# Kernel tuning notes

Hardware: AMD Instinct MI355X
Metric: run time of the kernel (lower is better)

## Reference

```python
import jax, jax.numpy as jnp
import numpy as np

N_NODES = 100000
IN_F = 256
OUT_F = 128
N_EDGES = 1600000


def setup_inputs() -> dict:
    key = jax.random.key(0)
    k1, k2, k3, k4 = jax.random.split(key, 4)
    inputs = jax.random.normal(k1, (N_NODES, IN_F), dtype=jnp.float32)
    edge = jax.random.randint(k2, (2, N_EDGES), 0, N_NODES, dtype=jnp.int64)
    # xavier_uniform for weight [in, out]
    bw = float(np.sqrt(6.0 / (IN_F + OUT_F)))
    weight = jax.random.uniform(k3, (IN_F, OUT_F), minval=-bw, maxval=bw, dtype=jnp.float32)
    ba = float(np.sqrt(6.0 / (OUT_F + 1)))
    a = jax.random.uniform(k4, (OUT_F, 1), minval=-ba, maxval=ba, dtype=jnp.float32)
    return {"inputs": inputs, "edge": edge, "weight": weight, "a": a}


def reference(inputs, edge, weight, a):
    # h: [N, out_features]
    h = inputs @ weight
    # edge-wise gather + abs-diff: [E, out_features]
    diff = jnp.abs(h[edge[0]] - h[edge[1]])
    # dot with attention vector a, relu, squeeze -> [E]
    edge_weight = jax.nn.relu((diff @ a).squeeze(-1))
    return (h, edge_weight)
```

## Files before the change

kernel.cpp:

```cpp
#include <hip/hip_runtime.h>
#include <hip/hip_bf16.h>
#include <stdint.h>

typedef __bf16 bf16x8 __attribute__((ext_vector_type(8)));
typedef float  f32x4  __attribute__((ext_vector_type(4)));

#define M_NODES 100000
#define K_IN    256
#define N_OUT   128
#define N_EDGE  1600000

template <bool FULL>
__device__ __forceinline__ void gemm_tile(
    const float* __restrict__ in, float* __restrict__ h,
    __hip_bfloat16* __restrict__ hmir,
    const bf16x8 (&bfrag)[8][2], const int m0, const int lr, const int q,
    const int nb)
{
    f32x4 acc[4][2];
    #pragma unroll
    for (int mt = 0; mt < 4; ++mt)
        #pragma unroll
        for (int nt = 0; nt < 2; ++nt)
            acc[mt][nt] = f32x4{0.f, 0.f, 0.f, 0.f};

    #pragma unroll
    for (int k8 = 0; k8 < 8; ++k8) {
        const int ka = k8 * 32 + q * 8;
        bf16x8 afrag[4];
        #pragma unroll
        for (int mt = 0; mt < 4; ++mt) {
            const int row = m0 + mt * 16 + lr;
            if (FULL || row < M_NODES) {
                const float* ap = in + (size_t)row * K_IN + ka;
                const f32x4 a0 = *(const f32x4*)ap;
                const f32x4 a1 = *(const f32x4*)(ap + 4);
                #pragma unroll
                for (int j = 0; j < 4; ++j) {
                    afrag[mt][j]     = (__bf16)a0[j];
                    afrag[mt][4 + j] = (__bf16)a1[j];
                }
            } else {
                #pragma unroll
                for (int j = 0; j < 8; ++j) afrag[mt][j] = (__bf16)0.f;
            }
        }
        #pragma unroll
        for (int mt = 0; mt < 4; ++mt)
            #pragma unroll
            for (int nt = 0; nt < 2; ++nt)
                acc[mt][nt] = __builtin_amdgcn_mfma_f32_16x16x32_bf16(
                    afrag[mt], bfrag[k8][nt], acc[mt][nt], 0, 0, 0);
    }

    #pragma unroll
    for (int mt = 0; mt < 4; ++mt) {
        const int rb = m0 + mt * 16 + q * 4;
        if (!FULL && rb >= M_NODES) continue;
        #pragma unroll
        for (int nt = 0; nt < 2; ++nt) {
            const int col = nb + nt * 16 + lr;
            #pragma unroll
            for (int r = 0; r < 4; ++r) {
                const float v = acc[mt][nt][r];
                __builtin_nontemporal_store(v, h + (size_t)(rb + r) * N_OUT + col);
                hmir[(size_t)(rb + r) * N_OUT + col] = __float2bfloat16(v);
            }
        }
    }
}

__global__ __launch_bounds__(256) void gemm_h_mfma(
    const float* __restrict__ in,
    const float* __restrict__ w,
    float* __restrict__ h,
    __hip_bfloat16* __restrict__ hmir)
{
    const int lane = threadIdx.x & 63;
    const int wave = threadIdx.x >> 6;
    const int nb   = wave * 32;
    const int lr   = lane & 15;
    const int q    = lane >> 4;

    bf16x8 bfrag[8][2];
    #pragma unroll
    for (int k8 = 0; k8 < 8; ++k8) {
        const int ka = k8 * 32 + q * 8;
        #pragma unroll
        for (int nt = 0; nt < 2; ++nt) {
            const int col = nb + nt * 16 + lr;
            #pragma unroll
            for (int j = 0; j < 8; ++j)
                bfrag[k8][nt][j] = (__bf16)w[(size_t)(ka + j) * N_OUT + col];
        }
    }

    const int ntiles = (M_NODES + 63) / 64;
    const int nfull  = M_NODES / 64;
    for (int t = blockIdx.x; t < ntiles; t += gridDim.x) {
        const int m0 = t * 64;
        if (t < nfull) gemm_tile<true >(in, h, hmir, bfrag, m0, lr, q, nb);
        else           gemm_tile<false>(in, h, hmir, bfrag, m0, lr, q, nb);
    }
}

__device__ inline int detect_i64(const uint32_t* p) {
    return __popcll(__ballot(p[2 * (threadIdx.x & 63) + 1] == 0u)) >= 60;
}

__global__ __launch_bounds__(256) void edge_kernel_bf16(
    const __hip_bfloat16* __restrict__ hm,
    const uint32_t* __restrict__ edge_raw,
    const float* __restrict__ a,
    float* __restrict__ ew,
    int E)
{
    const int e64 = detect_i64(edge_raw);
    const int s  = threadIdx.x & 15;
    const int g  = (int)((blockIdx.x * 256 + threadIdx.x) >> 4);
    const int e0 = g * 4;
    if (e0 >= E) return;

    const __bf16* hb = (const __bf16*)hm;
    const f32x4 a0 = *(const f32x4*)(a + s * 8);
    const f32x4 a1 = *(const f32x4*)(a + s * 8 + 4);

    if (e0 + 3 < E) {
        int srcs[4], dsts[4];
        if (e64) {
            const uint4 s01 = *(const uint4*)(edge_raw + 2 * (size_t)e0);
            const uint4 s23 = *(const uint4*)(edge_raw + 2 * (size_t)e0 + 4);
            const uint4 d01 = *(const uint4*)(edge_raw + 2 * ((size_t)E + e0));
            const uint4 d23 = *(const uint4*)(edge_raw + 2 * ((size_t)E + e0) + 4);
            srcs[0] = (int)s01.x; srcs[1] = (int)s01.z;
            srcs[2] = (int)s23.x; srcs[3] = (int)s23.z;
            dsts[0] = (int)d01.x; dsts[1] = (int)d01.z;
            dsts[2] = (int)d23.x; dsts[3] = (int)d23.z;
        } else {
            const int4 sv = *(const int4*)((const int*)edge_raw + e0);
            const int4 dv = *(const int4*)((const int*)edge_raw + (size_t)E + e0);
            srcs[0] = sv.x; srcs[1] = sv.y; srcs[2] = sv.z; srcs[3] = sv.w;
            dsts[0] = dv.x; dsts[1] = dv.y; dsts[2] = dv.z; dsts[3] = dv.w;
        }

        bf16x8 hs[4], hd[4];
        #pragma unroll
        for (int u = 0; u < 4; ++u) {
            hs[u] = *(const bf16x8*)(hb + (size_t)srcs[u] * N_OUT + s * 8);
            hd[u] = *(const bf16x8*)(hb + (size_t)dsts[u] * N_OUT + s * 8);
        }

        f32x4 rr;
        #pragma unroll
        for (int u = 0; u < 4; ++u) {
            float sum = 0.f;
            #pragma unroll
            for (int i = 0; i < 4; ++i)
                sum += fabsf((float)hs[u][i] - (float)hd[u][i]) * a0[i];
            #pragma unroll
            for (int i = 0; i < 4; ++i)
                sum += fabsf((float)hs[u][4 + i] - (float)hd[u][4 + i]) * a1[i];
            sum += __shfl_xor(sum, 1, 64);
            sum += __shfl_xor(sum, 2, 64);
            sum += __shfl_xor(sum, 4, 64);
            sum += __shfl_xor(sum, 8, 64);
            rr[u] = fmaxf(sum, 0.f);
        }
        if (s == 0) *(f32x4*)(ew + e0) = rr;
    } else {
        for (int e = e0; e < E; ++e) {
            int src, dst;
            if (e64) {
                src = (int)edge_raw[2 * (size_t)e];
                dst = (int)edge_raw[2 * ((size_t)E + e)];
            } else {
                const int* e32 = (const int*)edge_raw;
                src = e32[e];
                dst = e32[(size_t)E + e];
            }
            const bf16x8 hs = *(const bf16x8*)(hb + (size_t)src * N_OUT + s * 8);
            const bf16x8 hd = *(const bf16x8*)(hb + (size_t)dst * N_OUT + s * 8);
            float sum = 0.f;
            #pragma unroll
            for (int i = 0; i < 4; ++i)
                sum += fabsf((float)hs[i] - (float)hd[i]) * a0[i];
            #pragma unroll
            for (int i = 0; i < 4; ++i)
                sum += fabsf((float)hs[4 + i] - (float)hd[4 + i]) * a1[i];
            sum += __shfl_xor(sum, 1, 64);
            sum += __shfl_xor(sum, 2, 64);
            sum += __shfl_xor(sum, 4, 64);
            sum += __shfl_xor(sum, 8, 64);
            if (s == 0) ew[e] = fmaxf(sum, 0.f);
        }
    }
}

__global__ __launch_bounds__(256) void edge_kernel_f32(
    const float* __restrict__ h,
    const uint32_t* __restrict__ edge_raw,
    const float* __restrict__ a,
    float* __restrict__ ew,
    int E)
{
    const int e64 = detect_i64(edge_raw);
    const int s = threadIdx.x & 15;
    const int e = (int)((blockIdx.x * 256 + threadIdx.x) >> 4);
    if (e >= E) return;

    int src, dst;
    if (e64) {
        src = (int)edge_raw[2 * (size_t)e];
        dst = (int)edge_raw[2 * ((size_t)E + e)];
    } else {
        const int* e32 = (const int*)edge_raw;
        src = e32[e];
        dst = e32[(size_t)E + e];
    }

    const f32x4 s0 = *(const f32x4*)(h + (size_t)src * N_OUT + s * 8);
    const f32x4 s1 = *(const f32x4*)(h + (size_t)src * N_OUT + s * 8 + 4);
    const f32x4 d0 = *(const f32x4*)(h + (size_t)dst * N_OUT + s * 8);
    const f32x4 d1 = *(const f32x4*)(h + (size_t)dst * N_OUT + s * 8 + 4);
    const f32x4 a0 = *(const f32x4*)(a + s * 8);
    const f32x4 a1 = *(const f32x4*)(a + s * 8 + 4);

    float sum = 0.f;
    #pragma unroll
    for (int i = 0; i < 4; ++i) sum += fabsf(s0[i] - d0[i]) * a0[i];
    #pragma unroll
    for (int i = 0; i < 4; ++i) sum += fabsf(s1[i] - d1[i]) * a1[i];

    sum += __shfl_xor(sum, 1, 64);
    sum += __shfl_xor(sum, 2, 64);
    sum += __shfl_xor(sum, 4, 64);
    sum += __shfl_xor(sum, 8, 64);

    if (s == 0) ew[e] = fmaxf(sum, 0.f);
}

extern "C" void kernel_launch(void* const* d_in, const int* in_sizes, int n_in,
                              void* d_out, int out_size, void* d_ws, size_t ws_size,
                              hipStream_t stream) {
    const float*    in   = (const float*)d_in[0];
    const uint32_t* edge = (const uint32_t*)d_in[1];
    const float*    w    = (const float*)d_in[2];
    const float*    a    = (const float*)d_in[3];

    float* h  = (float*)d_out;
    float* ew = h + (size_t)M_NODES * N_OUT;

    const size_t mirror_bytes = (size_t)M_NODES * N_OUT * sizeof(__hip_bfloat16);
    __hip_bfloat16* hmir =
        (ws_size >= mirror_bytes) ? (__hip_bfloat16*)d_ws : nullptr;

    if (hmir) {
        gemm_h_mfma<<<dim3(1024), dim3(256), 0, stream>>>(in, w, h, hmir);
        const int egroups = (N_EDGE + 3) / 4;
        const int eblocks = (egroups * 16 + 255) / 256;
        edge_kernel_bf16<<<dim3(eblocks), dim3(256), 0, stream>>>(
            hmir, edge, a, ew, N_EDGE);
    } else {
        gemm_h_mfma<<<dim3(1024), dim3(256), 0, stream>>>(
            in, w, h, (__hip_bfloat16*)d_ws);
        const int eblocks = (N_EDGE * 16 + 255) / 256;
        edge_kernel_f32<<<dim3(eblocks), dim3(256), 0, stream>>>(
            h, edge, a, ew, N_EDGE);
    }
}
```

Baseline: 301.4 us.

## Stage GEMM A tile in swizzled LDS as bf16 shared across waves

Each 64-row input tile is now loaded cooperatively once by the whole block, converted to bf16 and written to shared memory with an XOR swizzle. The MFMA A fragments are then read from LDS instead of each of the four waves reloading the same fp32 rows from global memory. This cuts redundant global or L2 traffic and conversion work by roughly a factor of four. In exchange it uses 32KB of LDS per block, adds two barriers per tile, and has no double buffering, so loads and MFMA do not overlap.

```diff
diff --git a/kernel.cpp b/kernel.cpp
--- a/kernel.cpp
+++ b/kernel.cpp
@@ -4,6 +4,7 @@
 
 typedef __bf16 bf16x8 __attribute__((ext_vector_type(8)));
 typedef float  f32x4  __attribute__((ext_vector_type(4)));
+typedef short  s16x4  __attribute__((ext_vector_type(4)));
 
 #define M_NODES 100000
 #define K_IN    256
@@ -11,12 +12,29 @@
 #define N_EDGE  1600000
 
 template <bool FULL>
-__device__ __forceinline__ void gemm_tile(
+__device__ __forceinline__ void gemm_tile_lds(
     const float* __restrict__ in, float* __restrict__ h,
-    __hip_bfloat16* __restrict__ hmir,
-    const bf16x8 (&bfrag)[8][2], const int m0, const int lr, const int q,
-    const int nb)
-{
+    __hip_bfloat16* __restrict__ hmir, short* __restrict__ smA,
+    const bf16x8 (&bfrag)[8][2], const int m0, const int t,
+    const int lr, const int q, const int nb)
+{
+    #pragma unroll
+    for (int i = 0; i < 16; ++i) {
+        const int idx = i * 256 + t;
+        const int row = idx >> 6;
+        const int kc  = (idx & 63) * 4;
+        f32x4 v = f32x4{0.f, 0.f, 0.f, 0.f};
+        if (FULL || (m0 + row) < M_NODES)
+            v = *(const f32x4*)(in + (size_t)(m0 + row) * K_IN + kc);
+        s16x4 p;
+        #pragma unroll
+        for (int j = 0; j < 4; ++j)
+            p[j] = __builtin_bit_cast(short, (__bf16)v[j]);
+        const int byte = (row * 512 + kc * 2) ^ ((row & 7) << 4);
+        *(s16x4*)((char*)smA + byte) = p;
+    }
+    __syncthreads();
+
     f32x4 acc[4][2];
     #pragma unroll
     for (int mt = 0; mt < 4; ++mt)
@@ -26,24 +44,12 @@
 
     #pragma unroll
     for (int k8 = 0; k8 < 8; ++k8) {
-        const int ka = k8 * 32 + q * 8;
         bf16x8 afrag[4];
         #pragma unroll
         for (int mt = 0; mt < 4; ++mt) {
-            const int row = m0 + mt * 16 + lr;
-            if (FULL || row < M_NODES) {
-                const float* ap = in + (size_t)row * K_IN + ka;
-                const f32x4 a0 = *(const f32x4*)ap;
-                const f32x4 a1 = *(const f32x4*)(ap + 4);
-                #pragma unroll
-                for (int j = 0; j < 4; ++j) {
-                    afrag[mt][j]     = (__bf16)a0[j];
-                    afrag[mt][4 + j] = (__bf16)a1[j];
-                }
-            } else {
-                #pragma unroll
-                for (int j = 0; j < 8; ++j) afrag[mt][j] = (__bf16)0.f;
-            }
+            const int row  = mt * 16 + lr;
+            const int byte = (row * 512 + k8 * 64 + q * 16) ^ ((row & 7) << 4);
+            afrag[mt] = *(const bf16x8*)((const char*)smA + byte);
         }
         #pragma unroll
         for (int mt = 0; mt < 4; ++mt)
@@ -68,6 +74,7 @@
             }
         }
     }
+    __syncthreads();
 }
 
 __global__ __launch_bounds__(256) void gemm_h_mfma(
@@ -76,8 +83,11 @@
     float* __restrict__ h,
     __hip_bfloat16* __restrict__ hmir)
 {
-    const int lane = threadIdx.x & 63;
-    const int wave = threadIdx.x >> 6;
+    __shared__ __align__(16) short smA[64 * 256];
+
+    const int t    = threadIdx.x;
+    const int lane = t & 63;
+    const int wave = t >> 6;
     const int nb   = wave * 32;
     const int lr   = lane & 15;
     const int q    = lane >> 4;
@@ -97,10 +107,12 @@
 
     const int ntiles = (M_NODES + 63) / 64;
     const int nfull  = M_NODES / 64;
-    for (int t = blockIdx.x; t < ntiles; t += gridDim.x) {
-        const int m0 = t * 64;
-        if (t < nfull) gemm_tile<true >(in, h, hmir, bfrag, m0, lr, q, nb);
-        else           gemm_tile<false>(in, h, hmir, bfrag, m0, lr, q, nb);
+    for (int tt = blockIdx.x; tt < ntiles; tt += gridDim.x) {
+        const int m0 = tt * 64;
+        if (tt < nfull)
+            gemm_tile_lds<true >(in, h, hmir, smA, bfrag, m0, t, lr, q, nb);
+        else
+            gemm_tile_lds<false>(in, h, hmir, smA, bfrag, m0, t, lr, q, nb);
     }
 }
 
```

After: 317.4 us. +5.3%, slower.

## Stage bf16 weights in swizzled LDS and give each wave full-width row tiles

Applied to the files above, without the earlier changes.

The GEMM no longer keeps a per-wave slice of the weight matrix in registers. The whole weight matrix is converted to bf16 once per block and stored in LDS with an XOR swizzle, and each wave now computes a 16-row by 128-column tile. Each input row is loaded by only one wave instead of being reloaded by all four, which cuts redundant global and L2 traffic on the activations. The cost is 64KB of LDS per block, which limits occupancy, so the persistent grid is halved to 512 blocks. B fragments are now read from LDS inside the inner loop instead of coming from registers.

```diff
diff --git a/kernel.cpp b/kernel.cpp
--- a/kernel.cpp
+++ b/kernel.cpp
@@ -9,66 +9,6 @@
 #define K_IN    256
 #define N_OUT   128
 #define N_EDGE  1600000
-
-template <bool FULL>
-__device__ __forceinline__ void gemm_tile(
-    const float* __restrict__ in, float* __restrict__ h,
-    __hip_bfloat16* __restrict__ hmir,
-    const bf16x8 (&bfrag)[8][2], const int m0, const int lr, const int q,
-    const int nb)
-{
-    f32x4 acc[4][2];
-    #pragma unroll
-    for (int mt = 0; mt < 4; ++mt)
-        #pragma unroll
-        for (int nt = 0; nt < 2; ++nt)
-            acc[mt][nt] = f32x4{0.f, 0.f, 0.f, 0.f};
-
-    #pragma unroll
-    for (int k8 = 0; k8 < 8; ++k8) {
-        const int ka = k8 * 32 + q * 8;
-        bf16x8 afrag[4];
-        #pragma unroll
-        for (int mt = 0; mt < 4; ++mt) {
-            const int row = m0 + mt * 16 + lr;
-            if (FULL || row < M_NODES) {
-                const float* ap = in + (size_t)row * K_IN + ka;
-                const f32x4 a0 = *(const f32x4*)ap;
-                const f32x4 a1 = *(const f32x4*)(ap + 4);
-                #pragma unroll
-                for (int j = 0; j < 4; ++j) {
-                    afrag[mt][j]     = (__bf16)a0[j];
-                    afrag[mt][4 + j] = (__bf16)a1[j];
-                }
-            } else {
-                #pragma unroll
-                for (int j = 0; j < 8; ++j) afrag[mt][j] = (__bf16)0.f;
-            }
-        }
-        #pragma unroll
-        for (int mt = 0; mt < 4; ++mt)
-            #pragma unroll
-            for (int nt = 0; nt < 2; ++nt)
-                acc[mt][nt] = __builtin_amdgcn_mfma_f32_16x16x32_bf16(
-                    afrag[mt], bfrag[k8][nt], acc[mt][nt], 0, 0, 0);
-    }
-
-    #pragma unroll
-    for (int mt = 0; mt < 4; ++mt) {
-        const int rb = m0 + mt * 16 + q * 4;
-        if (!FULL && rb >= M_NODES) continue;
-        #pragma unroll
-        for (int nt = 0; nt < 2; ++nt) {
-            const int col = nb + nt * 16 + lr;
-            #pragma unroll
-            for (int r = 0; r < 4; ++r) {
-                const float v = acc[mt][nt][r];
-                __builtin_nontemporal_store(v, h + (size_t)(rb + r) * N_OUT + col);
-                hmir[(size_t)(rb + r) * N_OUT + col] = __float2bfloat16(v);
-            }
-        }
-    }
-}
 
 __global__ __launch_bounds__(256) void gemm_h_mfma(
     const float* __restrict__ in,
@@ -76,31 +16,76 @@
     float* __restrict__ h,
     __hip_bfloat16* __restrict__ hmir)
 {
-    const int lane = threadIdx.x & 63;
-    const int wave = threadIdx.x >> 6;
-    const int nb   = wave * 32;
+    __shared__ __align__(16) short smW[K_IN * N_OUT];
+
+    const int t    = threadIdx.x;
+    const int lane = t & 63;
+    const int wv   = t >> 6;
     const int lr   = lane & 15;
     const int q    = lane >> 4;
 
-    bf16x8 bfrag[8][2];
     #pragma unroll
-    for (int k8 = 0; k8 < 8; ++k8) {
-        const int ka = k8 * 32 + q * 8;
-        #pragma unroll
-        for (int nt = 0; nt < 2; ++nt) {
-            const int col = nb + nt * 16 + lr;
-            #pragma unroll
-            for (int j = 0; j < 8; ++j)
-                bfrag[k8][nt][j] = (__bf16)w[(size_t)(ka + j) * N_OUT + col];
-        }
-    }
+    for (int i = 0; i < 32; ++i) {
+        const int slot = i * 256 + t;
+        const int k    = slot >> 5;
+        const int c0   = (slot & 31) * 4;
+        const f32x4 v  = *(const f32x4*)(w + (size_t)k * N_OUT + c0);
+        const int kb   = (k >> 5) * 8192 + ((k >> 3) & 3) * 256 + (k & 7) * 2;
+        #pragma unroll
+        for (int j = 0; j < 4; ++j) {
+            const int c    = c0 + j;
+            const int nt   = c >> 4;
+            const int byte = kb + nt * 1024 + (((c & 15) * 16) ^ (nt << 4));
+            *(short*)((char*)smW + byte) =
+                __builtin_bit_cast(short, (__bf16)v[j]);
+        }
+    }
+    __syncthreads();
 
     const int ntiles = (M_NODES + 63) / 64;
-    const int nfull  = M_NODES / 64;
-    for (int t = blockIdx.x; t < ntiles; t += gridDim.x) {
-        const int m0 = t * 64;
-        if (t < nfull) gemm_tile<true >(in, h, hmir, bfrag, m0, lr, q, nb);
-        else           gemm_tile<false>(in, h, hmir, bfrag, m0, lr, q, nb);
+    for (int tt = blockIdx.x; tt < ntiles; tt += gridDim.x) {
+        const int mr = tt * 64 + wv * 16;
+        if (mr + 16 > M_NODES) continue;
+
+        const int   row = mr + lr;
+        const float* ap = in + (size_t)row * K_IN;
+
+        f32x4 acc[8];
+        #pragma unroll
+        for (int nt = 0; nt < 8; ++nt) acc[nt] = f32x4{0.f, 0.f, 0.f, 0.f};
+
+        #pragma unroll
+        for (int k8 = 0; k8 < 8; ++k8) {
+            const int ka = k8 * 32 + q * 8;
+            const f32x4 a0 = *(const f32x4*)(ap + ka);
+            const f32x4 a1 = *(const f32x4*)(ap + ka + 4);
+            bf16x8 afrag;
+            #pragma unroll
+            for (int j = 0; j < 4; ++j) {
+                afrag[j]     = (__bf16)a0[j];
+                afrag[4 + j] = (__bf16)a1[j];
+            }
+            const int kbase = k8 * 8192 + q * 256;
+            #pragma unroll
+            for (int nt = 0; nt < 8; ++nt) {
+                const int byte = kbase + nt * 1024 + ((lr * 16) ^ (nt << 4));
+                const bf16x8 bfrag = *(const bf16x8*)((const char*)smW + byte);
+                acc[nt] = __builtin_amdgcn_mfma_f32_16x16x32_bf16(
+                    afrag, bfrag, acc[nt], 0, 0, 0);
+            }
+        }
+
+        const int rb = mr + q * 4;
+        #pragma unroll
+        for (int nt = 0; nt < 8; ++nt) {
+            const int col = nt * 16 + lr;
+            #pragma unroll
+            for (int r = 0; r < 4; ++r) {
+                const float v = acc[nt][r];
+                __builtin_nontemporal_store(v, h + (size_t)(rb + r) * N_OUT + col);
+                hmir[(size_t)(rb + r) * N_OUT + col] = __float2bfloat16(v);
+            }
+        }
     }
 }
 
@@ -255,13 +240,13 @@
         (ws_size >= mirror_bytes) ? (__hip_bfloat16*)d_ws : nullptr;
 
     if (hmir) {
-        gemm_h_mfma<<<dim3(1024), dim3(256), 0, stream>>>(in, w, h, hmir);
+        gemm_h_mfma<<<dim3(512), dim3(256), 0, stream>>>(in, w, h, hmir);
         const int egroups = (N_EDGE + 3) / 4;
         const int eblocks = (egroups * 16 + 255) / 256;
         edge_kernel_bf16<<<dim3(eblocks), dim3(256), 0, stream>>>(
             hmir, edge, a, ew, N_EDGE);
     } else {
-        gemm_h_mfma<<<dim3(1024), dim3(256), 0, stream>>>(
+        gemm_h_mfma<<<dim3(512), dim3(256), 0, stream>>>(
             in, w, h, (__hip_bfloat16*)d_ws);
         const int eblocks = (N_EDGE * 16 + 255) / 256;
         edge_kernel_f32<<<dim3(eblocks), dim3(256), 0, stream>>>(
```

Result: faster. 288.5 us (-4.3%).
